# Kernel optimization log

Measured on AMD Instinct MI355X. Metric: run time of the kernel, lower is better.

The kernel has to match this reference:

```python
import jax, jax.numpy as jnp
import numpy as np

B, C, H, W = 8, 256, 48, 48
EPS = 1e-5


def setup_inputs() -> dict:
    key = jax.random.key(0)
    ks = jax.random.split(key, 14)
    n = lambda k, shape, s=1.0: jax.random.normal(k, shape, dtype=jnp.float32) * s
    return {
        "fea_left": n(ks[0], (B, C, H, W)),
        "fea_right": n(ks[1], (B, C, H, W)),
        # query branch: conv1x1 weight (out,in), bias, BN gamma/beta/running_mean/running_var
        "Wq": n(ks[2], (C, C), 0.05), "bq": n(ks[3], (C,), 0.05),
        "gq": 1.0 + n(ks[4], (C,), 0.05), "betaq": n(ks[5], (C,), 0.05),
        "mq": n(ks[6], (C,), 0.05),
        "vq": jax.random.uniform(ks[7], (C,), dtype=jnp.float32, minval=0.5, maxval=1.5),
        # key branch
        "Wk": n(ks[8], (C, C), 0.05), "bk": n(ks[9], (C,), 0.05),
        "gk": 1.0 + n(ks[10], (C,), 0.05), "betak": n(ks[11], (C,), 0.05),
        "mk": n(ks[12], (C,), 0.05),
        "vk": jax.random.uniform(ks[13], (C,), dtype=jnp.float32, minval=0.5, maxval=1.5),
    }


def _proj(x, Wt, b, g, beta, m, v):
    # conv1x1 (bias=True) followed by eval-mode BatchNorm2d
    y = jnp.einsum("bchw,oc->bohw", x, Wt) + b[:, None, None]
    scale = g * jax.lax.rsqrt(v + EPS)
    return (y - m[:, None, None]) * scale[:, None, None] + beta[:, None, None]


def reference(fea_left, fea_right, Wq, bq, gq, betaq, mq, vq, Wk, bk, gk, betak, mk, vk):
    b, c, h, w = fea_left.shape

    def attend(qsrc, ksrc, vsrc):
        # torch .view(b,-1,c): raw row-major reinterpretation -> plain reshape
        Q = _proj(qsrc, Wq, bq, gq, betaq, mq, vq).reshape(b, -1, c)  # (b, h*w, c)
        K = _proj(ksrc, Wk, bk, gk, betak, mk, vk).reshape(b, -1, c)
        A = jax.nn.softmax(jnp.einsum("bnc,bmc->bnm", Q, K) / c, axis=-1)
        out = jnp.einsum("bnm,bmc->bnc", A, vsrc.reshape(b, -1, c))
        return out.transpose(0, 2, 1).reshape(b, c, h, w)

    cxr = attend(fea_left, fea_right, fea_right)
    enh = attend(fea_right, fea_left, fea_left)
    return (cxr, enh)
```

## Files before the change

### kernel.cpp

```cpp
#include <hip/hip_runtime.h>

#define CH    256
#define NTOK  2304
#define MATSZ (CH * NTOK)

typedef __bf16 bf16x8 __attribute__((ext_vector_type(8)));
typedef float  f4v    __attribute__((ext_vector_type(4)));
typedef unsigned int u32x4 __attribute__((ext_vector_type(4)));

__device__ __forceinline__ unsigned short f2bf(float f) {
    union { float f; unsigned int i; } c;
    c.f = f;
    unsigned int x = c.i;
    x += 0x7fffu + ((x >> 16) & 1u);
    return (unsigned short)(x >> 16);
}

__device__ __forceinline__ bf16x8 cvt8(const float* p) {
    union { bf16x8 v; unsigned short s[8]; } u;
#pragma unroll
    for (int i = 0; i < 8; ++i) u.s[i] = f2bf(p[i]);
    return u.v;
}

__global__ __launch_bounds__(256) void tpose_k(
    const float* __restrict__ inL,
    const float* __restrict__ inR,
    unsigned short* __restrict__ out, int R, int Ccols)
{
    __shared__ unsigned short tile[64][72];
    int mat = blockIdx.y;
    const float* in = (mat >= 8 ? inR : inL) + (size_t)(mat & 7) * MATSZ;
    unsigned short* o = out + (size_t)mat * MATSZ;
    int tC = Ccols >> 6;
    int r0 = (blockIdx.x / tC) << 6;
    int c0 = (blockIdx.x % tC) << 6;
    int t = threadIdx.x;
    int col = t & 63, rs = t >> 6;
#pragma unroll
    for (int i = 0; i < 16; ++i) {
        int row = rs + i * 4;
        tile[row][col] = f2bf(in[(size_t)(r0 + row) * Ccols + c0 + col]);
    }
    __syncthreads();
#pragma unroll
    for (int i = 0; i < 16; ++i) {
        int crow = rs + i * 4;
        o[(size_t)(c0 + crow) * R + r0 + col] = tile[col][crow];
    }
}

__global__ __launch_bounds__(256, 2) void proj_k(
    const unsigned short* __restrict__ XT,
    const float* __restrict__ Wq_, const float* __restrict__ Wk_,
    const float* __restrict__ bq_, const float* __restrict__ bk_,
    const float* __restrict__ gq_, const float* __restrict__ gk_,
    const float* __restrict__ beq_, const float* __restrict__ bek_,
    const float* __restrict__ mq_, const float* __restrict__ mk_,
    const float* __restrict__ vq_, const float* __restrict__ vk_,
    unsigned short* __restrict__ Yout)
{
    __shared__ __align__(16) unsigned short Xs[64][264];
    int pb = blockIdx.y;
    int p = pb >> 3, b = pb & 7;
    int s = p & 1, br = p >> 1;
    const unsigned short* X = XT + (size_t)(s * 8 + b) * MATSZ;
    const float* W  = br ? Wk_ : Wq_;
    const float* bb = br ? bk_ : bq_;
    const float* gg = br ? gk_ : gq_;
    const float* be = br ? bek_ : beq_;
    const float* mm = br ? mk_ : mq_;
    const float* vv = br ? vk_ : vq_;
    unsigned short* Yo = Yout + (size_t)pb * MATSZ;

    int ot = blockIdx.x & 3, pt = blockIdx.x >> 2;
    int o0 = ot * 64, pos0 = pt * 64;
    int t = threadIdx.x;
    int w = t >> 6, lane = t & 63;
    int l15 = lane & 15, quad = lane >> 4;

    {
        int r = t >> 2, cq = (t & 3) << 6;
        const unsigned short* src = X + (size_t)(pos0 + r) * CH + cq;
        unsigned short* dst = &Xs[r][cq];
#pragma unroll
        for (int k = 0; k < 8; ++k)
            *(u32x4*)(dst + k * 8) = *(const u32x4*)(src + k * 8);
    }
    bf16x8 wf[8];
    {
        const float* wp = W + (size_t)(o0 + w * 16 + l15) * CH + quad * 8;
#pragma unroll
        for (int kc = 0; kc < 8; ++kc)
            wf[kc] = cvt8(wp + kc * 32);
    }
    __syncthreads();

    f4v zero4 = {0.f, 0.f, 0.f, 0.f};
    f4v acc[4] = {zero4, zero4, zero4, zero4};
#pragma unroll
    for (int kc = 0; kc < 8; ++kc) {
#pragma unroll
        for (int ct = 0; ct < 4; ++ct) {
            bf16x8 xb = *(const bf16x8*)(&Xs[ct * 16 + l15][kc * 32 + quad * 8]);
            acc[ct] = __builtin_amdgcn_mfma_f32_16x16x32_bf16(wf[kc], xb, acc[ct], 0, 0, 0);
        }
    }
#pragma unroll
    for (int r = 0; r < 4; ++r) {
        int o = o0 + w * 16 + quad * 4 + r;
        float scale = gg[o] * rsqrtf(vv[o] + 1e-5f);
        float shift = (bb[o] - mm[o]) * scale + be[o];
#pragma unroll
        for (int ct = 0; ct < 4; ++ct) {
            float val = acc[ct][r] * scale + shift;
            Yo[(size_t)o * NTOK + pos0 + ct * 16 + l15] = f2bf(val);
        }
    }
}

__global__ __launch_bounds__(256, 2) void attn_k(
    const unsigned short* __restrict__ Y,
    const unsigned short* __restrict__ VT,
    float* __restrict__ out)
{
    __shared__ __align__(16) unsigned short lds[16384 + 16384 + 4608];
    unsigned short* Ks = lds;
    unsigned short* Vs = lds + 16384;
    unsigned short* Ps = lds + 32768;

    int bid = blockIdx.x;
    int wg = (bid & 7) * 72 + (bid >> 3);
    int qt = wg % 36;
    int ab = wg / 36;
    int a = ab >> 3, b = ab & 7;
    const unsigned short* Qp = Y + (size_t)(a * 8 + b) * MATSZ;
    const unsigned short* Kp = Y + (size_t)((3 - a) * 8 + b) * MATSZ;
    const unsigned short* Vp = VT + (size_t)((1 - a) * 8 + b) * MATSZ;
    float* Op = out + (size_t)ab * MATSZ;

    int t = threadIdx.x;
    int w = t >> 6, lane = t & 63;
    int l15 = lane & 15, quad = lane >> 4;

    const unsigned short* ksrc0 = Kp + t * 8;
    const unsigned short* vsrc0 = Vp + (size_t)(t >> 3) * NTOK + ((t & 7) << 3);
    int kxor = ((t >> 5) & 7) << 4;
    int vxor = ((t >> 3) & 7) << 4;
    char* kdst = (char*)Ks + ((t * 16) ^ kxor);
    char* vdst = (char*)Vs + ((t * 16) ^ vxor);
    int rxor = (l15 & 7) << 4;

    bf16x8 qf[8];
    {
        const unsigned short* qp = Qp + (size_t)(qt * 64 + w * 16 + l15) * CH + quad * 8;
#pragma unroll
        for (int kc = 0; kc < 8; ++kc) qf[kc] = *(const bf16x8*)(qp + kc * 32);
    }
    f4v zero4 = {0.f, 0.f, 0.f, 0.f};
    f4v acc_o[16];
#pragma unroll
    for (int i = 0; i < 16; ++i) acc_o[i] = zero4;
    float l_acc[4] = {0.f, 0.f, 0.f, 0.f};
    __bf16* Pw = (__bf16*)(Ps + w * 16 * 72);

    u32x4 kreg[8], vreg[8];
#pragma unroll
    for (int k = 0; k < 8; ++k) kreg[k] = *(const u32x4*)(ksrc0 + k * 2048);
#pragma unroll
    for (int k = 0; k < 8; ++k) vreg[k] = *(const u32x4*)(vsrc0 + (size_t)k * 32 * NTOK);

    for (int kt = 0; kt < 36; ++kt) {
        __syncthreads();
#pragma unroll
        for (int k = 0; k < 8; ++k) *(u32x4*)(kdst + k * 4096) = kreg[k];
#pragma unroll
        for (int k = 0; k < 8; ++k) *(u32x4*)(vdst + k * 4096) = vreg[k];

        if (kt < 35) {
            const unsigned short* kn = ksrc0 + (size_t)(kt + 1) * 16384;
            const unsigned short* vn = vsrc0 + (size_t)(kt + 1) * 64;
#pragma unroll
            for (int k = 0; k < 8; ++k) kreg[k] = *(const u32x4*)(kn + k * 2048);
#pragma unroll
            for (int k = 0; k < 8; ++k) vreg[k] = *(const u32x4*)(vn + (size_t)k * 32 * NTOK);
        }
        __syncthreads();

        f4v accs[4] = {zero4, zero4, zero4, zero4};
#pragma unroll
        for (int kc = 0; kc < 8; ++kc) {
#pragma unroll
            for (int ct = 0; ct < 4; ++ct) {
                const char* kaddr = (const char*)Ks + ((ct * 16 + l15) << 9)
                                  + (((kc << 6) + (quad << 4)) ^ rxor);
                bf16x8 kf = *(const bf16x8*)kaddr;
                accs[ct] = __builtin_amdgcn_mfma_f32_16x16x32_bf16(qf[kc], kf, accs[ct], 0, 0, 0);
            }
        }
        float pv[4][4];
#pragma unroll
        for (int r = 0; r < 4; ++r) {
#pragma unroll
            for (int ct = 0; ct < 4; ++ct) {
                float pe = __expf(accs[ct][r] * (1.0f / 256.0f));
                pv[ct][r] = pe;
                l_acc[r] += pe;
            }
        }
#pragma unroll
        for (int r = 0; r < 4; ++r)
#pragma unroll
            for (int ct = 0; ct < 4; ++ct)
                Pw[(quad * 4 + r) * 72 + ct * 16 + l15] = (__bf16)pv[ct][r];
        __asm__ volatile("s_waitcnt lgkmcnt(0)" ::: "memory");
#pragma unroll
        for (int kc = 0; kc < 2; ++kc) {
            bf16x8 pf = *(const bf16x8*)(Pw + l15 * 72 + kc * 32 + quad * 8);
#pragma unroll
            for (int ct = 0; ct < 16; ++ct) {
                const char* vaddr = (const char*)Vs + ((ct * 16 + l15) << 7)
                                  + (((kc << 6) + (quad << 4)) ^ rxor);
                bf16x8 vf = *(const bf16x8*)vaddr;
                acc_o[ct] = __builtin_amdgcn_mfma_f32_16x16x32_bf16(pf, vf, acc_o[ct], 0, 0, 0);
            }
        }
    }

#pragma unroll
    for (int r = 0; r < 4; ++r) {
        float rs = l_acc[r];
        rs += __shfl_xor(rs, 1, 64);
        rs += __shfl_xor(rs, 2, 64);
        rs += __shfl_xor(rs, 4, 64);
        rs += __shfl_xor(rs, 8, 64);
        l_acc[r] = rs;
    }

    __syncthreads();
    float* Ot = (float*)lds;
#pragma unroll
    for (int ct = 0; ct < 16; ++ct)
#pragma unroll
        for (int r = 0; r < 4; ++r) {
            float val = acc_o[ct][r] / l_acc[r];
            Ot[(ct * 16 + l15) * 73 + (w * 16 + quad * 4 + r)] = val;
        }
    __syncthreads();
    for (int cg = 0; cg < 64; ++cg) {
        int c = cg * 4 + w;
        Op[(size_t)c * NTOK + qt * 64 + lane] = Ot[c * 73 + lane];
    }
}

extern "C" void kernel_launch(void* const* d_in, const int* in_sizes, int n_in,
                              void* d_out, int out_size, void* d_ws, size_t ws_size,
                              hipStream_t stream) {
    (void)in_sizes; (void)n_in; (void)out_size; (void)ws_size;
    const float* feaL  = (const float*)d_in[0];
    const float* feaR  = (const float*)d_in[1];
    const float* Wq    = (const float*)d_in[2];
    const float* bq    = (const float*)d_in[3];
    const float* gq    = (const float*)d_in[4];
    const float* betaq = (const float*)d_in[5];
    const float* mq    = (const float*)d_in[6];
    const float* vq    = (const float*)d_in[7];
    const float* Wk    = (const float*)d_in[8];
    const float* bk    = (const float*)d_in[9];
    const float* gk    = (const float*)d_in[10];
    const float* betak = (const float*)d_in[11];
    const float* mk    = (const float*)d_in[12];
    const float* vk    = (const float*)d_in[13];

    unsigned short* XT = (unsigned short*)d_ws;
    unsigned short* VT = XT;
    unsigned short* Yb = XT + (size_t)16 * MATSZ;
    float* out = (float*)d_out;

    dim3 blk(256);
    tpose_k<<<dim3(144, 16), blk, 0, stream>>>(feaL, feaR, XT, 256, 2304);
    proj_k<<<dim3(144, 32), blk, 0, stream>>>(XT, Wq, Wk, bq, bk, gq, gk,
                                              betaq, betak, mq, mk, vq, vk, Yb);
    tpose_k<<<dim3(144, 16), blk, 0, stream>>>(feaL, feaR, VT, 2304, 256);
    attn_k<<<dim3(576), blk, 0, stream>>>(Yb, VT, out);
}
```

Measured before the change: 359.9 us.

## Split attention work across waves by key tile and channel instead of query rows

The attention kernel now keeps the 64-query Q tile in LDS and gives each wave its own 16 keys per tile for QK^T and a 64-channel slice of V for PV. K and V fragments load straight from global memory into registers, so the K/V LDS staging and its register prefetch are gone. P is exchanged through a double-buffered, swizzled LDS buffer, and row sums are combined across waves through LDS. The output is written back in two halves. The change also raises launch bounds to 3 blocks per SM, trading latency hiding from explicit prefetch for more occupancy and less LDS traffic, at the cost of uncoalesced-ish direct global loads each iteration.

```diff
diff --git a/kernel.cpp b/kernel.cpp
--- a/kernel.cpp
+++ b/kernel.cpp
@@ -119,15 +119,15 @@
     }
 }
 
-__global__ __launch_bounds__(256, 2) void attn_k(
+__global__ __launch_bounds__(256, 3) void attn_k(
     const unsigned short* __restrict__ Y,
     const unsigned short* __restrict__ VT,
     float* __restrict__ out)
 {
-    __shared__ __align__(16) unsigned short lds[16384 + 16384 + 4608];
-    unsigned short* Ks = lds;
-    unsigned short* Vs = lds + 16384;
-    unsigned short* Ps = lds + 32768;
+    __shared__ __align__(16) unsigned char lds[50176];
+    unsigned char* Qs  = lds;
+    unsigned char* Pb0 = lds + 32768;
+    float*         Ls  = (float*)(lds + 49152);
 
     int bid = blockIdx.x;
     int wg = (bid & 7) * 72 + (bid >> 3);
@@ -142,114 +142,128 @@
     int t = threadIdx.x;
     int w = t >> 6, lane = t & 63;
     int l15 = lane & 15, quad = lane >> 4;
-
-    const unsigned short* ksrc0 = Kp + t * 8;
-    const unsigned short* vsrc0 = Vp + (size_t)(t >> 3) * NTOK + ((t & 7) << 3);
-    int kxor = ((t >> 5) & 7) << 4;
-    int vxor = ((t >> 3) & 7) << 4;
-    char* kdst = (char*)Ks + ((t * 16) ^ kxor);
-    char* vdst = (char*)Vs + ((t * 16) ^ vxor);
     int rxor = (l15 & 7) << 4;
 
-    bf16x8 qf[8];
     {
-        const unsigned short* qp = Qp + (size_t)(qt * 64 + w * 16 + l15) * CH + quad * 8;
-#pragma unroll
-        for (int kc = 0; kc < 8; ++kc) qf[kc] = *(const bf16x8*)(qp + kc * 32);
-    }
+        const unsigned short* qsrc = Qp + (size_t)qt * 64 * CH + t * 8;
+        int qxor = ((t >> 5) & 7) << 4;
+        unsigned char* qdst = Qs + ((t * 16) ^ qxor);
+#pragma unroll
+        for (int k = 0; k < 8; ++k)
+            *(u32x4*)(qdst + k * 4096) = *(const u32x4*)(qsrc + k * 2048);
+    }
+    __syncthreads();
+
     f4v zero4 = {0.f, 0.f, 0.f, 0.f};
-    f4v acc_o[16];
-#pragma unroll
-    for (int i = 0; i < 16; ++i) acc_o[i] = zero4;
-    float l_acc[4] = {0.f, 0.f, 0.f, 0.f};
-    __bf16* Pw = (__bf16*)(Ps + w * 16 * 72);
-
-    u32x4 kreg[8], vreg[8];
-#pragma unroll
-    for (int k = 0; k < 8; ++k) kreg[k] = *(const u32x4*)(ksrc0 + k * 2048);
-#pragma unroll
-    for (int k = 0; k < 8; ++k) vreg[k] = *(const u32x4*)(vsrc0 + (size_t)k * 32 * NTOK);
+    f4v acc_o[4][4];
+#pragma unroll
+    for (int f = 0; f < 4; ++f)
+#pragma unroll
+        for (int c = 0; c < 4; ++c) acc_o[f][c] = zero4;
+    float l_acc[4][4];
+#pragma unroll
+    for (int f = 0; f < 4; ++f)
+#pragma unroll
+        for (int r = 0; r < 4; ++r) l_acc[f][r] = 0.f;
+
+    const unsigned short* KpT = Kp + (size_t)(w * 16 + l15) * CH + quad * 8;
+    const unsigned short* VpT = Vp + (size_t)(w * 64 + l15) * NTOK + quad * 8;
 
     for (int kt = 0; kt < 36; ++kt) {
+        bf16x8 kf[8];
+        {
+            const unsigned short* kp = KpT + (size_t)kt * 64 * CH;
+#pragma unroll
+            for (int kc = 0; kc < 8; ++kc)
+                kf[kc] = *(const bf16x8*)(kp + kc * 32);
+        }
+        f4v accs[4] = {zero4, zero4, zero4, zero4};
+#pragma unroll
+        for (int kc = 0; kc < 8; ++kc) {
+#pragma unroll
+            for (int f = 0; f < 4; ++f) {
+                bf16x8 qa = *(const bf16x8*)(Qs + ((f * 16 + l15) << 9)
+                                           + (((kc << 6) + (quad << 4)) ^ rxor));
+                accs[f] = __builtin_amdgcn_mfma_f32_16x16x32_bf16(qa, kf[kc], accs[f], 0, 0, 0);
+            }
+        }
+        unsigned char* pb = Pb0 + ((kt & 1) << 13);
+#pragma unroll
+        for (int f = 0; f < 4; ++f)
+#pragma unroll
+            for (int r = 0; r < 4; ++r) {
+                float pe = __expf(accs[f][r] * (1.0f / 256.0f));
+                l_acc[f][r] += pe;
+                int q = f * 16 + quad * 4 + r;
+                *(__bf16*)(pb + q * 128 + ((w * 32 + l15 * 2) ^ ((q & 7) << 4))) = (__bf16)pe;
+            }
+        bf16x8 vf[4][2];
+        {
+            const unsigned short* vp = VpT + kt * 64;
+#pragma unroll
+            for (int ct2 = 0; ct2 < 4; ++ct2)
+#pragma unroll
+                for (int kc2 = 0; kc2 < 2; ++kc2)
+                    vf[ct2][kc2] = *(const bf16x8*)(vp + (size_t)ct2 * 16 * NTOK + kc2 * 32);
+        }
         __syncthreads();
 #pragma unroll
-        for (int k = 0; k < 8; ++k) *(u32x4*)(kdst + k * 4096) = kreg[k];
-#pragma unroll
-        for (int k = 0; k < 8; ++k) *(u32x4*)(vdst + k * 4096) = vreg[k];
-
-        if (kt < 35) {
-            const unsigned short* kn = ksrc0 + (size_t)(kt + 1) * 16384;
-            const unsigned short* vn = vsrc0 + (size_t)(kt + 1) * 64;
-#pragma unroll
-            for (int k = 0; k < 8; ++k) kreg[k] = *(const u32x4*)(kn + k * 2048);
-#pragma unroll
-            for (int k = 0; k < 8; ++k) vreg[k] = *(const u32x4*)(vn + (size_t)k * 32 * NTOK);
-        }
+        for (int kc2 = 0; kc2 < 2; ++kc2)
+#pragma unroll
+            for (int f = 0; f < 4; ++f) {
+                bf16x8 pf = *(const bf16x8*)(pb + ((f * 16 + l15) << 7)
+                                           + (((kc2 << 6) + (quad << 4)) ^ rxor));
+#pragma unroll
+                for (int ct2 = 0; ct2 < 4; ++ct2)
+                    acc_o[f][ct2] = __builtin_amdgcn_mfma_f32_16x16x32_bf16(pf, vf[ct2][kc2], acc_o[f][ct2], 0, 0, 0);
+            }
+    }
+
+#pragma unroll
+    for (int f = 0; f < 4; ++f)
+#pragma unroll
+        for (int r = 0; r < 4; ++r) {
+            float rs = l_acc[f][r];
+            rs += __shfl_xor(rs, 1, 64);
+            rs += __shfl_xor(rs, 2, 64);
+            rs += __shfl_xor(rs, 4, 64);
+            rs += __shfl_xor(rs, 8, 64);
+            int q = f * 16 + quad * 4 + r;
+            Ls[w * 64 + q] = rs;
+        }
+    __syncthreads();
+    float l_tot[4][4];
+#pragma unroll
+    for (int f = 0; f < 4; ++f)
+#pragma unroll
+        for (int r = 0; r < 4; ++r) {
+            int q = f * 16 + quad * 4 + r;
+            l_tot[f][r] = Ls[q] + Ls[64 + q] + Ls[128 + q] + Ls[192 + q];
+        }
+
+    float* Ot = (float*)lds;
+    for (int p = 0; p < 2; ++p) {
         __syncthreads();
-
-        f4v accs[4] = {zero4, zero4, zero4, zero4};
-#pragma unroll
-        for (int kc = 0; kc < 8; ++kc) {
-#pragma unroll
-            for (int ct = 0; ct < 4; ++ct) {
-                const char* kaddr = (const char*)Ks + ((ct * 16 + l15) << 9)
-                                  + (((kc << 6) + (quad << 4)) ^ rxor);
-                bf16x8 kf = *(const bf16x8*)kaddr;
-                accs[ct] = __builtin_amdgcn_mfma_f32_16x16x32_bf16(qf[kc], kf, accs[ct], 0, 0, 0);
-            }
-        }
-        float pv[4][4];
-#pragma unroll
-        for (int r = 0; r < 4; ++r) {
-#pragma unroll
-            for (int ct = 0; ct < 4; ++ct) {
-                float pe = __expf(accs[ct][r] * (1.0f / 256.0f));
-                pv[ct][r] = pe;
-                l_acc[r] += pe;
-            }
-        }
-#pragma unroll
-        for (int r = 0; r < 4; ++r)
-#pragma unroll
-            for (int ct = 0; ct < 4; ++ct)
-                Pw[(quad * 4 + r) * 72 + ct * 16 + l15] = (__bf16)pv[ct][r];
-        __asm__ volatile("s_waitcnt lgkmcnt(0)" ::: "memory");
-#pragma unroll
-        for (int kc = 0; kc < 2; ++kc) {
-            bf16x8 pf = *(const bf16x8*)(Pw + l15 * 72 + kc * 32 + quad * 8);
-#pragma unroll
-            for (int ct = 0; ct < 16; ++ct) {
-                const char* vaddr = (const char*)Vs + ((ct * 16 + l15) << 7)
-                                  + (((kc << 6) + (quad << 4)) ^ rxor);
-                bf16x8 vf = *(const bf16x8*)vaddr;
-                acc_o[ct] = __builtin_amdgcn_mfma_f32_16x16x32_bf16(pf, vf, acc_o[ct], 0, 0, 0);
-            }
-        }
-    }
-
-#pragma unroll
-    for (int r = 0; r < 4; ++r) {
-        float rs = l_acc[r];
-        rs += __shfl_xor(rs, 1, 64);
-        rs += __shfl_xor(rs, 2, 64);
-        rs += __shfl_xor(rs, 4, 64);
-        rs += __shfl_xor(rs, 8, 64);
-        l_acc[r] = rs;
-    }
-
-    __syncthreads();
-    float* Ot = (float*)lds;
-#pragma unroll
-    for (int ct = 0; ct < 16; ++ct)
-#pragma unroll
-        for (int r = 0; r < 4; ++r) {
-            float val = acc_o[ct][r] / l_acc[r];
-            Ot[(ct * 16 + l15) * 73 + (w * 16 + quad * 4 + r)] = val;
-        }
-    __syncthreads();
-    for (int cg = 0; cg < 64; ++cg) {
-        int c = cg * 4 + w;
-        Op[(size_t)c * NTOK + qt * 64 + lane] = Ot[c * 73 + lane];
+        if ((w >> 1) == p) {
+            int wl = w & 1;
+#pragma unroll
+            for (int f = 0; f < 4; ++f)
+#pragma unroll
+                for (int ct2 = 0; ct2 < 4; ++ct2)
+#pragma unroll
+                    for (int r = 0; r < 4; ++r) {
+                        float val = acc_o[f][ct2][r] / l_tot[f][r];
+                        int cl = wl * 64 + ct2 * 16 + l15;
+                        int q = f * 16 + quad * 4 + r;
+                        Ot[cl * 73 + q] = val;
+                    }
+        }
+        __syncthreads();
+        for (int cg = 0; cg < 32; ++cg) {
+            int cl = cg * 4 + w;
+            int c = p * 128 + cl;
+            Op[(size_t)c * NTOK + qt * 64 + lane] = Ot[cl * 73 + lane];
+        }
     }
 }
 
```

New measurement: 408.0 us. 13.4% more time.

## Restructure attention kernel to 32x32 MFMA tiles with direct global-to-LDS loads

Applied to the files above, without the earlier changes.

Rewrites the attention kernel so each wave computes a 32x32 QK tile using mfma_f32_32x32x16_bf16. The four waves split as two query halves by two key halves for QK, then two query halves by two channel halves for PV, and P is shared through LDS with a barrier. K/V tiles are now loaded with global_load_lds directly into LDS instead of register prefetch, removing the register double buffer but also the overlap of the next tile's loads with compute. Row sums are combined across waves via LDS, and the output transpose uses vectorized float4 writes with an XOR swizzle.

```diff
diff --git a/kernel.cpp b/kernel.cpp
--- a/kernel.cpp
+++ b/kernel.cpp
@@ -6,6 +6,7 @@
 
 typedef __bf16 bf16x8 __attribute__((ext_vector_type(8)));
 typedef float  f4v    __attribute__((ext_vector_type(4)));
+typedef float  f16v   __attribute__((ext_vector_type(16)));
 typedef unsigned int u32x4 __attribute__((ext_vector_type(4)));
 
 __device__ __forceinline__ unsigned short f2bf(float f) {
@@ -124,10 +125,11 @@
     const unsigned short* __restrict__ VT,
     float* __restrict__ out)
 {
-    __shared__ __align__(16) unsigned short lds[16384 + 16384 + 4608];
-    unsigned short* Ks = lds;
-    unsigned short* Vs = lds + 16384;
-    unsigned short* Ps = lds + 32768;
+    __shared__ __align__(16) unsigned char lds[74240];
+    unsigned char* Ks = lds;
+    unsigned char* Vs = lds + 32768;
+    unsigned char* Pb = lds + 65536;
+    float*         Ls = (float*)(lds + 73728);
 
     int bid = blockIdx.x;
     int wg = (bid & 7) * 72 + (bid >> 3);
@@ -141,115 +143,131 @@
 
     int t = threadIdx.x;
     int w = t >> 6, lane = t & 63;
-    int l15 = lane & 15, quad = lane >> 4;
-
-    const unsigned short* ksrc0 = Kp + t * 8;
-    const unsigned short* vsrc0 = Vp + (size_t)(t >> 3) * NTOK + ((t & 7) << 3);
-    int kxor = ((t >> 5) & 7) << 4;
-    int vxor = ((t >> 3) & 7) << 4;
-    char* kdst = (char*)Ks + ((t * 16) ^ kxor);
-    char* vdst = (char*)Vs + ((t * 16) ^ vxor);
-    int rxor = (l15 & 7) << 4;
-
-    bf16x8 qf[8];
+    int l31 = lane & 31, h = lane >> 5;
+    int qb = w >> 1;
+    int kb = w & 1;
+    int chh = w & 1;
+    int rxor = (l31 & 7) << 4;
+
+    const unsigned char* kS = (const unsigned char*)Kp
+        + ((t * 16) ^ (((t >> 5) & 7) << 4));
+    const unsigned char* vS = (const unsigned char*)Vp
+        + (size_t)(t >> 3) * 4608
+        + (((t & 7) * 16) ^ (((t >> 3) & 7) << 4));
+    unsigned char* kD = Ks + t * 16;
+    unsigned char* vD = Vs + t * 16;
+
+    bf16x8 qf[16];
     {
-        const unsigned short* qp = Qp + (size_t)(qt * 64 + w * 16 + l15) * CH + quad * 8;
-#pragma unroll
-        for (int kc = 0; kc < 8; ++kc) qf[kc] = *(const bf16x8*)(qp + kc * 32);
-    }
-    f4v zero4 = {0.f, 0.f, 0.f, 0.f};
-    f4v acc_o[16];
-#pragma unroll
-    for (int i = 0; i < 16; ++i) acc_o[i] = zero4;
-    float l_acc[4] = {0.f, 0.f, 0.f, 0.f};
-    __bf16* Pw = (__bf16*)(Ps + w * 16 * 72);
-
-    u32x4 kreg[8], vreg[8];
-#pragma unroll
-    for (int k = 0; k < 8; ++k) kreg[k] = *(const u32x4*)(ksrc0 + k * 2048);
-#pragma unroll
-    for (int k = 0; k < 8; ++k) vreg[k] = *(const u32x4*)(vsrc0 + (size_t)k * 32 * NTOK);
+        const unsigned short* qp = Qp + (size_t)(qt * 64 + qb * 32 + l31) * CH + h * 8;
+#pragma unroll
+        for (int ks = 0; ks < 16; ++ks)
+            qf[ks] = *(const bf16x8*)(qp + ks * 16);
+    }
+
+    f16v acc_o[4];
+#pragma unroll
+    for (int c = 0; c < 4; ++c)
+#pragma unroll
+        for (int r = 0; r < 16; ++r) acc_o[c][r] = 0.f;
+    float l_acc[16];
+#pragma unroll
+    for (int r = 0; r < 16; ++r) l_acc[r] = 0.f;
 
     for (int kt = 0; kt < 36; ++kt) {
         __syncthreads();
 #pragma unroll
-        for (int k = 0; k < 8; ++k) *(u32x4*)(kdst + k * 4096) = kreg[k];
-#pragma unroll
-        for (int k = 0; k < 8; ++k) *(u32x4*)(vdst + k * 4096) = vreg[k];
-
-        if (kt < 35) {
-            const unsigned short* kn = ksrc0 + (size_t)(kt + 1) * 16384;
-            const unsigned short* vn = vsrc0 + (size_t)(kt + 1) * 64;
-#pragma unroll
-            for (int k = 0; k < 8; ++k) kreg[k] = *(const u32x4*)(kn + k * 2048);
-#pragma unroll
-            for (int k = 0; k < 8; ++k) vreg[k] = *(const u32x4*)(vn + (size_t)k * 32 * NTOK);
-        }
+        for (int k = 0; k < 8; ++k)
+            __builtin_amdgcn_global_load_lds(
+                (const unsigned int*)(kS + (size_t)kt * 32768 + k * 4096),
+                (unsigned int*)(kD + k * 4096), 16, 0, 0);
+#pragma unroll
+        for (int k = 0; k < 8; ++k)
+            __builtin_amdgcn_global_load_lds(
+                (const unsigned int*)(vS + (size_t)kt * 128 + (size_t)k * 147456),
+                (unsigned int*)(vD + k * 4096), 16, 0, 0);
         __syncthreads();
 
-        f4v accs[4] = {zero4, zero4, zero4, zero4};
-#pragma unroll
-        for (int kc = 0; kc < 8; ++kc) {
-#pragma unroll
-            for (int ct = 0; ct < 4; ++ct) {
-                const char* kaddr = (const char*)Ks + ((ct * 16 + l15) << 9)
-                                  + (((kc << 6) + (quad << 4)) ^ rxor);
-                bf16x8 kf = *(const bf16x8*)kaddr;
-                accs[ct] = __builtin_amdgcn_mfma_f32_16x16x32_bf16(qf[kc], kf, accs[ct], 0, 0, 0);
+        f16v accs;
+#pragma unroll
+        for (int r = 0; r < 16; ++r) accs[r] = 0.f;
+        const unsigned char* krow = Ks + ((kb * 32 + l31) << 9);
+#pragma unroll
+        for (int ks = 0; ks < 16; ++ks) {
+            bf16x8 kf = *(const bf16x8*)(krow + ((ks * 32 + h * 16) ^ rxor));
+            accs = __builtin_amdgcn_mfma_f32_32x32x16_bf16(qf[ks], kf, accs, 0, 0, 0);
+        }
+#pragma unroll
+        for (int r = 0; r < 16; ++r) {
+            float pe = __expf(accs[r] * (1.0f / 256.0f));
+            l_acc[r] += pe;
+            int row = (r & 3) + 8 * (r >> 2) + 4 * h;
+            int q = qb * 32 + row;
+            *(__bf16*)(Pb + q * 128 + ((kb * 64 + l31 * 2) ^ ((row & 7) << 4))) = (__bf16)pe;
+        }
+        __syncthreads();
+
+#pragma unroll
+        for (int ks2 = 0; ks2 < 4; ++ks2) {
+            bf16x8 pf = *(const bf16x8*)(Pb + ((qb * 32 + l31) << 7)
+                                       + ((ks2 * 32 + h * 16) ^ rxor));
+#pragma unroll
+            for (int chb = 0; chb < 4; ++chb) {
+                int ch = chh * 128 + chb * 32 + l31;
+                bf16x8 vf = *(const bf16x8*)(Vs + (ch << 7)
+                                           + ((ks2 * 32 + h * 16) ^ rxor));
+                acc_o[chb] = __builtin_amdgcn_mfma_f32_32x32x16_bf16(pf, vf, acc_o[chb], 0, 0, 0);
             }
         }
-        float pv[4][4];
-#pragma unroll
-        for (int r = 0; r < 4; ++r) {
-#pragma unroll
-            for (int ct = 0; ct < 4; ++ct) {
-                float pe = __expf(accs[ct][r] * (1.0f / 256.0f));
-                pv[ct][r] = pe;
-                l_acc[r] += pe;
-            }
-        }
-#pragma unroll
-        for (int r = 0; r < 4; ++r)
-#pragma unroll
-            for (int ct = 0; ct < 4; ++ct)
-                Pw[(quad * 4 + r) * 72 + ct * 16 + l15] = (__bf16)pv[ct][r];
-        __asm__ volatile("s_waitcnt lgkmcnt(0)" ::: "memory");
-#pragma unroll
-        for (int kc = 0; kc < 2; ++kc) {
-            bf16x8 pf = *(const bf16x8*)(Pw + l15 * 72 + kc * 32 + quad * 8);
-#pragma unroll
-            for (int ct = 0; ct < 16; ++ct) {
-                const char* vaddr = (const char*)Vs + ((ct * 16 + l15) << 7)
-                                  + (((kc << 6) + (quad << 4)) ^ rxor);
-                bf16x8 vf = *(const bf16x8*)vaddr;
-                acc_o[ct] = __builtin_amdgcn_mfma_f32_16x16x32_bf16(pf, vf, acc_o[ct], 0, 0, 0);
-            }
-        }
-    }
-
-#pragma unroll
-    for (int r = 0; r < 4; ++r) {
+    }
+
+#pragma unroll
+    for (int r = 0; r < 16; ++r) {
         float rs = l_acc[r];
         rs += __shfl_xor(rs, 1, 64);
         rs += __shfl_xor(rs, 2, 64);
         rs += __shfl_xor(rs, 4, 64);
         rs += __shfl_xor(rs, 8, 64);
+        rs += __shfl_xor(rs, 16, 64);
         l_acc[r] = rs;
     }
-
+    if (l31 == 0) {
+#pragma unroll
+        for (int r = 0; r < 16; ++r) {
+            int row = (r & 3) + 8 * (r >> 2) + 4 * h;
+            Ls[w * 32 + row] = l_acc[r];
+        }
+    }
     __syncthreads();
+    float l_tot[16];
+#pragma unroll
+    for (int r = 0; r < 16; ++r) {
+        int row = (r & 3) + 8 * (r >> 2) + 4 * h;
+        l_tot[r] = Ls[w * 32 + row] + Ls[(w ^ 1) * 32 + row];
+    }
+
     float* Ot = (float*)lds;
 #pragma unroll
-    for (int ct = 0; ct < 16; ++ct)
-#pragma unroll
-        for (int r = 0; r < 4; ++r) {
-            float val = acc_o[ct][r] / l_acc[r];
-            Ot[(ct * 16 + l15) * 73 + (w * 16 + quad * 4 + r)] = val;
-        }
+    for (int chb = 0; chb < 4; ++chb) {
+        int c = chh * 128 + chb * 32 + l31;
+        int cx = (c & 7) << 2;
+#pragma unroll
+        for (int rr = 0; rr < 4; ++rr) {
+            f4v v4;
+#pragma unroll
+            for (int i = 0; i < 4; ++i)
+                v4[i] = acc_o[chb][rr * 4 + i] / l_tot[rr * 4 + i];
+            int q0 = qb * 32 + rr * 8 + h * 4;
+            *(f4v*)(Ot + c * 64 + (q0 ^ cx)) = v4;
+        }
+    }
     __syncthreads();
-    for (int cg = 0; cg < 64; ++cg) {
-        int c = cg * 4 + w;
-        Op[(size_t)c * NTOK + qt * 64 + lane] = Ot[c * 73 + lane];
+#pragma unroll
+    for (int p = 0; p < 16; ++p) {
+        int c = p * 16 + (t >> 4);
+        int q = (t & 15) * 4;
+        f4v v4 = *(const f4v*)(Ot + c * 64 + (q ^ ((c & 7) << 2)));
+        *(f4v*)(Op + (size_t)c * NTOK + qt * 64 + q) = v4;
     }
 }
 
```

Result: faster. 340.2 us (-5.5%).
